# Optimization experiments

Measured on AMD Instinct MI355X. Metric: run time of the kernel, lower is better.

The kernel has to match this reference:

```python
import jax, jax.numpy as jnp
import numpy as np

C = 256
CQK = C // 8


def setup_inputs() -> dict:
    key = jax.random.key(0)
    ks = jax.random.split(key, 8)
    B, H, W = 4, 64, 64
    inputs = jax.random.normal(ks[0], (B, H, W, C), dtype=jnp.float32)
    s = 1.0 / np.sqrt(C)
    Wq = jax.random.normal(ks[1], (C, CQK), dtype=jnp.float32) * s
    bq = jnp.zeros((CQK,), dtype=jnp.float32)
    Wk = jax.random.normal(ks[2], (C, CQK), dtype=jnp.float32) * s
    bk = jnp.zeros((CQK,), dtype=jnp.float32)
    Wv = jax.random.normal(ks[3], (C, C), dtype=jnp.float32) * s
    bv = jnp.zeros((C,), dtype=jnp.float32)
    gamma = jnp.float32(0.7)  # nonzero so attention branch contributes
    return {"inputs": inputs, "Wq": Wq, "bq": bq, "Wk": Wk, "bk": bk,
            "Wv": Wv, "bv": bv, "gamma": gamma}


def reference(inputs, Wq, bq, Wk, bk, Wv, bv, gamma):
    B, H, W, Cin = inputs.shape
    N = H * W
    x = inputs.reshape(B, N, Cin)
    # 1x1 convs == per-pixel channel matmuls
    q = x @ Wq + bq                      # (B, N, C//8)
    k = x @ Wk + bk                      # (B, N, C//8)
    v = x @ Wv + bv                      # (B, N, C)
    energy = jnp.einsum('bnd,bmd->bnm', q, k)   # (B, N, N), no scale (faithful)
    attn = jax.nn.softmax(energy, axis=-1)
    x_out = jnp.einsum('bnm,bmc->bnc', attn, v)  # (B, N, C)
    out = gamma * x_out.reshape(B, H, W, Cin) + inputs
    return out
```

## Files before the change

### kernel.cpp

```cpp
#include <hip/hip_runtime.h>
#include <hip/hip_bf16.h>

#define B_ 4
#define N_ 4096
#define C_ 256
#define D_ 32
#define LOG2E 1.44269504088896340736f

typedef __attribute__((ext_vector_type(8))) short short8;
typedef __attribute__((ext_vector_type(4))) short short4v;
typedef __attribute__((ext_vector_type(4))) float float4v;

__device__ inline short f2bf_rne(float f) {
  unsigned u = __builtin_bit_cast(unsigned, f);
  u += 0x7FFFu + ((u >> 16) & 1u);
  return (short)(u >> 16);
}

__device__ inline float fast_exp2(float x) { return __builtin_amdgcn_exp2f(x); }

__global__ __launch_bounds__(256) void cast_w_kernel(
    const float* __restrict__ Wq, const float* __restrict__ Wk,
    const float* __restrict__ Wv, short* __restrict__ WtF) {
  int i  = blockIdx.x * 256 + threadIdx.x;
  int j  = i & 7;
  int l  = (i >> 3) & 63;
  int ks = (i >> 9) & 7;
  int nb = i >> 12;
  int n  = nb * 16 + (l & 15);
  int k  = ks * 32 + ((l >> 4) << 3) + j;
  float v;
  if (n < 32)      v = Wq[k * 32 + n] * LOG2E;
  else if (n < 64) v = Wk[k * 32 + (n - 32)];
  else             v = Wv[k * 256 + (n - 64)];
  WtF[i] = f2bf_rne(v);
}

__global__ __launch_bounds__(256, 2) void proj_kernel(
    const float* __restrict__ x, const short* __restrict__ WtF,
    const float* __restrict__ bq, const float* __restrict__ bk,
    const float* __restrict__ bv,
    short* __restrict__ qb, short* __restrict__ kF, short* __restrict__ vF) {
  int blk = blockIdx.x;
  int b  = blk >> 7;
  int r0 = (blk & 127) * 32;
  int t  = threadIdx.x;
  int w  = t >> 6;
  int l  = t & 63;
  int lc = l & 15;
  int q4 = l >> 4;

  __shared__ __align__(16) short sA[32][272];
  __shared__ __align__(16) short sV[256][40];
  __shared__ __align__(16) short sK[32][36];

  {
    const float* xb = x + (size_t)(b * N_ + r0) * C_;
#pragma unroll
    for (int ch = 0; ch < 8; ch++) {
      int f   = ch * 256 + t;
      int row = f >> 6;
      int col = (f & 63) * 4;
      float4v v = *(const float4v*)(xb + f * 4);
      short4v s;
      s[0] = f2bf_rne(v[0]); s[1] = f2bf_rne(v[1]);
      s[2] = f2bf_rne(v[2]); s[3] = f2bf_rne(v[3]);
      *(short4v*)(&sA[row][col]) = s;
    }
  }
  __syncthreads();

  float4v acc[10];
#pragma unroll
  for (int i = 0; i < 10; i++) { acc[i][0] = 0.f; acc[i][1] = 0.f; acc[i][2] = 0.f; acc[i][3] = 0.f; }

#pragma unroll
  for (int ks = 0; ks < 8; ks++) {
    short8 af0 = *(const short8*)(&sA[lc][ks * 32 + q4 * 8]);
    short8 af1 = *(const short8*)(&sA[16 + lc][ks * 32 + q4 * 8]);
#pragma unroll
    for (int nbo = 0; nbo < 5; nbo++) {
      int nb = w * 5 + nbo;
      short8 bf = *(const short8*)(WtF + (((nb << 3) + ks) << 9) + l * 8);
      acc[nbo * 2 + 0] = __builtin_amdgcn_mfma_f32_16x16x32_bf16(af0, bf, acc[nbo * 2 + 0], 0, 0, 0);
      acc[nbo * 2 + 1] = __builtin_amdgcn_mfma_f32_16x16x32_bf16(af1, bf, acc[nbo * 2 + 1], 0, 0, 0);
    }
  }

#pragma unroll
  for (int nbo = 0; nbo < 5; nbo++) {
    int n = (w * 5 + nbo) * 16 + lc;
    float bias = (n < 32) ? bq[n] * LOG2E : (n < 64) ? bk[n - 32] : bv[n - 64];
#pragma unroll
    for (int rt = 0; rt < 2; rt++) {
#pragma unroll
      for (int r = 0; r < 4; r++) {
        int row = rt * 16 + q4 * 4 + r;
        short s = f2bf_rne(acc[nbo * 2 + rt][r] + bias);
        if (n < 32)      qb[(size_t)(b * N_ + r0 + row) * D_ + n] = s;
        else if (n < 64) sK[row][n - 32] = s;
        else             sV[n - 64][row] = s;
      }
    }
  }
  __syncthreads();

  int kt  = r0 >> 6;
  int ks0 = (r0 >> 5) & 1;

  {
    int c = t;
    size_t tb = ((size_t)(b * 64 + kt) * 32 + ks0 * 16 + (c >> 4)) * 512;
#pragma unroll
    for (int rg = 0; rg < 4; rg++) {
      short8 vv = *(const short8*)(&sV[c][rg * 8]);
      *(short8*)(vF + tb + (rg * 16 + (c & 15)) * 8) = vv;
    }
  }
  if (t < 128) {
    int row = t >> 2, dg = t & 3;
    size_t tb = ((size_t)(b * 64 + kt) * 4 + ks0 * 2 + (row >> 4)) * 512;
    short8 kv = *(const short8*)(&sK[row][dg * 8]);
    *(short8*)(kF + tb + (dg * 16 + (row & 15)) * 8) = kv;
  }
}

__global__ __launch_bounds__(512, 2) void flash_kernel(
    const short* __restrict__ qb, const short* __restrict__ kF,
    const short* __restrict__ vF, const float* __restrict__ xin,
    const float* __restrict__ gptr, float* __restrict__ out) {
  int blk = blockIdx.x;
  int b  = blk & 3;
  int qt = (blk >> 3) * 2 + ((blk >> 2) & 1);
  int r0 = qt * 64;
  int t  = threadIdx.x;
  int w  = t >> 6;
  int l  = t & 63;
  int lc = l & 15;
  int q4 = l >> 4;
  int rq = w & 3;
  int h  = w >> 2;

  __shared__ __align__(16) short sP[8][16][36];
  __shared__ __align__(16) float4v mbuf[2][16][64];
  __shared__ float sLh[64];
  __shared__ float sLm[64];

  short8 qf = *(const short8*)(qb + (size_t)(b * N_ + r0 + rq * 16 + lc) * D_ + q4 * 8);

  const short* kp = kF + (size_t)b * (64 * 4 * 512) + h * (2 * 512) + l * 8;
  const short* vp = vF + (size_t)b * (64 * 32 * 512) + h * (16 * 512) + l * 8;

  short8 vA[16], vB[16];
  short8 kX0, kX1, kY0, kY1;

  kX0 = *(const short8*)(kp);
  kX1 = *(const short8*)(kp + 512);
#pragma unroll
  for (int cb = 0; cb < 16; cb++)
    vA[cb] = *(const short8*)(vp + cb * 512);

  float4v O[16];
#pragma unroll
  for (int i = 0; i < 16; i++) { O[i][0] = 0.f; O[i][1] = 0.f; O[i][2] = 0.f; O[i][3] = 0.f; }
  float l_part = 0.f;

  short (*sPw)[36] = sP[w];

#define TILE_PHASE(KC0, KC1, KP0, KP1, VCUR, VNXT, TI)                          \
  {                                                                             \
    int nt = ((TI) + 1 < 64) ? (TI) + 1 : 63;                                   \
    _Pragma("unroll")                                                           \
    for (int cb = 0; cb < 16; cb++)                                             \
      VNXT[cb] = *(const short8*)(vp + (size_t)nt * (32 * 512) + cb * 512);     \
    KP0 = *(const short8*)(kp + (size_t)nt * (4 * 512));                        \
    KP1 = *(const short8*)(kp + (size_t)nt * (4 * 512) + 512);                  \
    float4v z; z[0] = 0.f; z[1] = 0.f; z[2] = 0.f; z[3] = 0.f;                  \
    float4v St0 = __builtin_amdgcn_mfma_f32_16x16x32_bf16(KC0, qf, z, 0, 0, 0); \
    float4v St1 = __builtin_amdgcn_mfma_f32_16x16x32_bf16(KC1, qf, z, 0, 0, 0); \
    float p0 = fast_exp2(St0[0]), p1 = fast_exp2(St0[1]);                       \
    float p2 = fast_exp2(St0[2]), p3 = fast_exp2(St0[3]);                       \
    float p4 = fast_exp2(St1[0]), p5 = fast_exp2(St1[1]);                       \
    float p6 = fast_exp2(St1[2]), p7 = fast_exp2(St1[3]);                       \
    l_part += ((p0 + p1) + (p2 + p3)) + ((p4 + p5) + (p6 + p7));                \
    short4v pk0, pk1;                                                           \
    pk0[0] = f2bf_rne(p0); pk0[1] = f2bf_rne(p1);                               \
    pk0[2] = f2bf_rne(p2); pk0[3] = f2bf_rne(p3);                               \
    pk1[0] = f2bf_rne(p4); pk1[1] = f2bf_rne(p5);                               \
    pk1[2] = f2bf_rne(p6); pk1[3] = f2bf_rne(p7);                               \
    *(short4v*)(&sPw[lc][q4 * 4]) = pk0;                                        \
    *(short4v*)(&sPw[lc][16 + q4 * 4]) = pk1;                                   \
    short8 pf = *(const short8*)(&sPw[lc][q4 * 8]);                             \
    _Pragma("unroll")                                                           \
    for (int cb = 0; cb < 16; cb++)                                             \
      O[cb] = __builtin_amdgcn_mfma_f32_16x16x32_bf16(pf, VCUR[cb], O[cb], 0, 0, 0); \
  }

  for (int kt = 0; kt < 64; kt += 2) {
    TILE_PHASE(kX0, kX1, kY0, kY1, vA, vB, kt);
    TILE_PHASE(kY0, kY1, kX0, kX1, vB, vA, kt + 1);
  }
#undef TILE_PHASE

  float l_tot = l_part + __shfl_xor(l_part, 16, 64);
  l_tot += __shfl_xor(l_tot, 32, 64);
  bool lo = (h == 0);
  if (!lo && q4 == 0) sLh[rq * 16 + lc] = l_tot;
  __syncthreads();
  if (lo && q4 == 0) sLm[rq * 16 + lc] = l_tot + sLh[rq * 16 + lc];

  if (w == 4 || w == 5) {
#pragma unroll
    for (int cb = 0; cb < 16; cb++) mbuf[w - 4][cb][l] = O[cb];
  }
  __syncthreads();
  if (w == 0 || w == 1) {
#pragma unroll
    for (int cb = 0; cb < 16; cb++) {
      float4v m = mbuf[w][cb][l];
      O[cb][0] += m[0]; O[cb][1] += m[1]; O[cb][2] += m[2]; O[cb][3] += m[3];
    }
  }
  __syncthreads();
  if (w == 6 || w == 7) {
#pragma unroll
    for (int cb = 0; cb < 16; cb++) mbuf[w - 6][cb][l] = O[cb];
  }
  __syncthreads();
  if (w == 2 || w == 3) {
#pragma unroll
    for (int cb = 0; cb < 16; cb++) {
      float4v m = mbuf[w - 2][cb][l];
      O[cb][0] += m[0]; O[cb][1] += m[1]; O[cb][2] += m[2]; O[cb][3] += m[3];
    }
  }

  if (lo) {
    float g = *gptr;
    float4v lv = *(const float4v*)(&sLm[rq * 16 + q4 * 4]);
    float4v inv;
#pragma unroll
    for (int r = 0; r < 4; r++) inv[r] = __builtin_amdgcn_rcpf(lv[r]);
#pragma unroll
    for (int cb = 0; cb < 16; cb++) {
#pragma unroll
      for (int r = 0; r < 4; r++) {
        size_t idx = (size_t)(b * N_ + r0 + rq * 16 + q4 * 4 + r) * C_ + cb * 16 + lc;
        out[idx] = g * (O[cb][r] * inv[r]) + xin[idx];
      }
    }
  }
}

extern "C" void kernel_launch(void* const* d_in, const int* in_sizes, int n_in,
                              void* d_out, int out_size, void* d_ws, size_t ws_size,
                              hipStream_t stream) {
  const float* x     = (const float*)d_in[0];
  const float* Wq    = (const float*)d_in[1];
  const float* bq    = (const float*)d_in[2];
  const float* Wk    = (const float*)d_in[3];
  const float* bk    = (const float*)d_in[4];
  const float* Wv    = (const float*)d_in[5];
  const float* bv    = (const float*)d_in[6];
  const float* gamma = (const float*)d_in[7];
  float* out = (float*)d_out;

  char* ws = (char*)d_ws;
  short* qb  = (short*)ws;
  short* kF  = (short*)(ws + (1u << 20));
  short* vF  = (short*)(ws + (2u << 20));
  short* WtF = (short*)(ws + (10u << 20));

  hipLaunchKernelGGL(cast_w_kernel, dim3(320), dim3(256), 0, stream, Wq, Wk, Wv, WtF);
  hipLaunchKernelGGL(proj_kernel,   dim3(512), dim3(256), 0, stream, x, WtF, bq, bk, bv, qb, kF, vF);
  hipLaunchKernelGGL(flash_kernel,  dim3(256), dim3(512), 0, stream, qb, kF, vF, x, gamma, out);
}
```

Baseline: 164.6 us.

## Split flash attention over key halves with partial outputs and a merge kernel

Restructures attention so each block handles a 64-query tile over half of the keys. Score computation is shared through a double-buffered LDS P tile by four waves, while eight waves split the V columns and key sub-blocks. Partial outputs and row sums go to workspace in bf16, and a new merge kernel combines the halves and applies gamma plus the residual. This doubles the grid and cuts per-thread V register prefetch so occupancy can rise (launch bounds raised to 4). The cost is an extra kernel launch, a global round-trip of the partials, per-tile block barriers, and bf16 rounding of intermediate sums. It also reorders the proj_kernel column-block assignment per wave.

```diff
diff --git a/kernel.cpp b/kernel.cpp
--- a/kernel.cpp
+++ b/kernel.cpp
@@ -16,7 +16,10 @@
   u += 0x7FFFu + ((u >> 16) & 1u);
   return (short)(u >> 16);
 }
-
+__device__ inline float bf2f(short s) {
+  unsigned u = ((unsigned)(unsigned short)s) << 16;
+  return __builtin_bit_cast(float, u);
+}
 __device__ inline float fast_exp2(float x) { return __builtin_amdgcn_exp2f(x); }
 
 __global__ __launch_bounds__(256) void cast_w_kernel(
@@ -36,7 +39,7 @@
   WtF[i] = f2bf_rne(v);
 }
 
-__global__ __launch_bounds__(256, 2) void proj_kernel(
+__global__ __launch_bounds__(256, 4) void proj_kernel(
     const float* __restrict__ x, const short* __restrict__ WtF,
     const float* __restrict__ bq, const float* __restrict__ bk,
     const float* __restrict__ bv,
@@ -80,7 +83,7 @@
     short8 af1 = *(const short8*)(&sA[16 + lc][ks * 32 + q4 * 8]);
 #pragma unroll
     for (int nbo = 0; nbo < 5; nbo++) {
-      int nb = w * 5 + nbo;
+      int nb = nbo * 4 + w;
       short8 bf = *(const short8*)(WtF + (((nb << 3) + ks) << 9) + l * 8);
       acc[nbo * 2 + 0] = __builtin_amdgcn_mfma_f32_16x16x32_bf16(af0, bf, acc[nbo * 2 + 0], 0, 0, 0);
       acc[nbo * 2 + 1] = __builtin_amdgcn_mfma_f32_16x16x32_bf16(af1, bf, acc[nbo * 2 + 1], 0, 0, 0);
@@ -89,17 +92,21 @@
 
 #pragma unroll
   for (int nbo = 0; nbo < 5; nbo++) {
-    int n = (w * 5 + nbo) * 16 + lc;
-    float bias = (n < 32) ? bq[n] * LOG2E : (n < 64) ? bk[n - 32] : bv[n - 64];
+    float bias;
+    if (nbo == 0) bias = (w < 2) ? bq[w * 16 + lc] * LOG2E : bk[(w - 2) * 16 + lc];
+    else          bias = bv[(nbo - 1) * 64 + w * 16 + lc];
 #pragma unroll
     for (int rt = 0; rt < 2; rt++) {
 #pragma unroll
       for (int r = 0; r < 4; r++) {
         int row = rt * 16 + q4 * 4 + r;
         short s = f2bf_rne(acc[nbo * 2 + rt][r] + bias);
-        if (n < 32)      qb[(size_t)(b * N_ + r0 + row) * D_ + n] = s;
-        else if (n < 64) sK[row][n - 32] = s;
-        else             sV[n - 64][row] = s;
+        if (nbo == 0) {
+          if (w < 2) qb[(size_t)(b * N_ + r0 + row) * D_ + w * 16 + lc] = s;
+          else       sK[row][(w - 2) * 16 + lc] = s;
+        } else {
+          sV[(nbo - 1) * 64 + w * 16 + lc][row] = s;
+        }
       }
     }
   }
@@ -125,13 +132,14 @@
   }
 }
 
-__global__ __launch_bounds__(512, 2) void flash_kernel(
+__global__ __launch_bounds__(512, 4) void flash_partial_kernel(
     const short* __restrict__ qb, const short* __restrict__ kF,
-    const short* __restrict__ vF, const float* __restrict__ xin,
-    const float* __restrict__ gptr, float* __restrict__ out) {
+    const short* __restrict__ vF, short* __restrict__ obuf,
+    float* __restrict__ lbuf) {
   int blk = blockIdx.x;
   int b  = blk & 3;
-  int qt = (blk >> 3) * 2 + ((blk >> 2) & 1);
+  int hb = (blk >> 2) & 1;
+  int qt = blk >> 3;
   int r0 = qt * 64;
   int t  = threadIdx.x;
   int w  = t >> 6;
@@ -139,116 +147,184 @@
   int lc = l & 15;
   int q4 = l >> 4;
   int rq = w & 3;
-  int h  = w >> 2;
-
-  __shared__ __align__(16) short sP[8][16][36];
-  __shared__ __align__(16) float4v mbuf[2][16][64];
-  __shared__ float sLh[64];
-  __shared__ float sLm[64];
+  int kh = w >> 2;
+  int cq = w & 3;
+
+  __shared__ __align__(16) short sP[2][64][72];
+
+  int p = (b * 64 + qt) * 2 + hb;
 
   short8 qf = *(const short8*)(qb + (size_t)(b * N_ + r0 + rq * 16 + lc) * D_ + q4 * 8);
 
-  const short* kp = kF + (size_t)b * (64 * 4 * 512) + h * (2 * 512) + l * 8;
-  const short* vp = vF + (size_t)b * (64 * 32 * 512) + h * (16 * 512) + l * 8;
-
-  short8 vA[16], vB[16];
-  short8 kX0, kX1, kY0, kY1;
-
-  kX0 = *(const short8*)(kp);
-  kX1 = *(const short8*)(kp + 512);
-#pragma unroll
-  for (int cb = 0; cb < 16; cb++)
-    vA[cb] = *(const short8*)(vp + cb * 512);
+  const short* kpb = kF + ((size_t)(b * 64 + hb * 32) * 4) * 512 + l * 8;
+  const short* vpb = vF + ((size_t)(b * 64 + hb * 32) * 32 + kh * 16 + cq * 4) * 512 + l * 8;
+
+  short8 kr0, kr1, kr2, kr3;
+  short8 vr0, vr1, vr2, vr3;
+  kr0 = *(const short8*)(kpb + 0 * 512);
+  kr1 = *(const short8*)(kpb + 1 * 512);
+  kr2 = *(const short8*)(kpb + 2 * 512);
+  kr3 = *(const short8*)(kpb + 3 * 512);
+  vr0 = *(const short8*)(vpb + 0 * 512);
+  vr1 = *(const short8*)(vpb + 1 * 512);
+  vr2 = *(const short8*)(vpb + 2 * 512);
+  vr3 = *(const short8*)(vpb + 3 * 512);
 
   float4v O[16];
 #pragma unroll
   for (int i = 0; i < 16; i++) { O[i][0] = 0.f; O[i][1] = 0.f; O[i][2] = 0.f; O[i][3] = 0.f; }
   float l_part = 0.f;
 
-  short (*sPw)[36] = sP[w];
-
-#define TILE_PHASE(KC0, KC1, KP0, KP1, VCUR, VNXT, TI)                          \
-  {                                                                             \
-    int nt = ((TI) + 1 < 64) ? (TI) + 1 : 63;                                   \
-    _Pragma("unroll")                                                           \
-    for (int cb = 0; cb < 16; cb++)                                             \
-      VNXT[cb] = *(const short8*)(vp + (size_t)nt * (32 * 512) + cb * 512);     \
-    KP0 = *(const short8*)(kp + (size_t)nt * (4 * 512));                        \
-    KP1 = *(const short8*)(kp + (size_t)nt * (4 * 512) + 512);                  \
-    float4v z; z[0] = 0.f; z[1] = 0.f; z[2] = 0.f; z[3] = 0.f;                  \
-    float4v St0 = __builtin_amdgcn_mfma_f32_16x16x32_bf16(KC0, qf, z, 0, 0, 0); \
-    float4v St1 = __builtin_amdgcn_mfma_f32_16x16x32_bf16(KC1, qf, z, 0, 0, 0); \
-    float p0 = fast_exp2(St0[0]), p1 = fast_exp2(St0[1]);                       \
-    float p2 = fast_exp2(St0[2]), p3 = fast_exp2(St0[3]);                       \
-    float p4 = fast_exp2(St1[0]), p5 = fast_exp2(St1[1]);                       \
-    float p6 = fast_exp2(St1[2]), p7 = fast_exp2(St1[3]);                       \
-    l_part += ((p0 + p1) + (p2 + p3)) + ((p4 + p5) + (p6 + p7));                \
-    short4v pk0, pk1;                                                           \
-    pk0[0] = f2bf_rne(p0); pk0[1] = f2bf_rne(p1);                               \
-    pk0[2] = f2bf_rne(p2); pk0[3] = f2bf_rne(p3);                               \
-    pk1[0] = f2bf_rne(p4); pk1[1] = f2bf_rne(p5);                               \
-    pk1[2] = f2bf_rne(p6); pk1[3] = f2bf_rne(p7);                               \
-    *(short4v*)(&sPw[lc][q4 * 4]) = pk0;                                        \
-    *(short4v*)(&sPw[lc][16 + q4 * 4]) = pk1;                                   \
-    short8 pf = *(const short8*)(&sPw[lc][q4 * 8]);                             \
-    _Pragma("unroll")                                                           \
-    for (int cb = 0; cb < 16; cb++)                                             \
-      O[cb] = __builtin_amdgcn_mfma_f32_16x16x32_bf16(pf, VCUR[cb], O[cb], 0, 0, 0); \
-  }
-
-  for (int kt = 0; kt < 64; kt += 2) {
-    TILE_PHASE(kX0, kX1, kY0, kY1, vA, vB, kt);
-    TILE_PHASE(kY0, kY1, kX0, kX1, vB, vA, kt + 1);
-  }
-#undef TILE_PHASE
-
-  float l_tot = l_part + __shfl_xor(l_part, 16, 64);
-  l_tot += __shfl_xor(l_tot, 32, 64);
-  bool lo = (h == 0);
-  if (!lo && q4 == 0) sLh[rq * 16 + lc] = l_tot;
-  __syncthreads();
-  if (lo && q4 == 0) sLm[rq * 16 + lc] = l_tot + sLh[rq * 16 + lc];
-
+  for (int ti = 0; ti < 32; ti++) {
+    short* sPb = &sP[ti & 1][0][0];
+    size_t nto = (size_t)((ti + 1 < 32) ? ti + 1 : 31);
+
+    if (w < 4) {
+      float4v z; z[0] = 0.f; z[1] = 0.f; z[2] = 0.f; z[3] = 0.f;
+      float4v St0 = __builtin_amdgcn_mfma_f32_16x16x32_bf16(kr0, qf, z, 0, 0, 0);
+      float4v St1 = __builtin_amdgcn_mfma_f32_16x16x32_bf16(kr1, qf, z, 0, 0, 0);
+      float4v St2 = __builtin_amdgcn_mfma_f32_16x16x32_bf16(kr2, qf, z, 0, 0, 0);
+      float4v St3 = __builtin_amdgcn_mfma_f32_16x16x32_bf16(kr3, qf, z, 0, 0, 0);
+      kr0 = *(const short8*)(kpb + nto * 2048 + 0 * 512);
+      kr1 = *(const short8*)(kpb + nto * 2048 + 1 * 512);
+      kr2 = *(const short8*)(kpb + nto * 2048 + 2 * 512);
+      kr3 = *(const short8*)(kpb + nto * 2048 + 3 * 512);
+      short* rowp = sPb + (rq * 16 + lc) * 72 + q4 * 4;
+      float ts;
+      {
+        float p0 = fast_exp2(St0[0]), p1 = fast_exp2(St0[1]);
+        float p2 = fast_exp2(St0[2]), p3 = fast_exp2(St0[3]);
+        ts = (p0 + p1) + (p2 + p3);
+        short4v pk; pk[0] = f2bf_rne(p0); pk[1] = f2bf_rne(p1);
+        pk[2] = f2bf_rne(p2); pk[3] = f2bf_rne(p3);
+        *(short4v*)(rowp + 0) = pk;
+      }
+      {
+        float p0 = fast_exp2(St1[0]), p1 = fast_exp2(St1[1]);
+        float p2 = fast_exp2(St1[2]), p3 = fast_exp2(St1[3]);
+        ts += (p0 + p1) + (p2 + p3);
+        short4v pk; pk[0] = f2bf_rne(p0); pk[1] = f2bf_rne(p1);
+        pk[2] = f2bf_rne(p2); pk[3] = f2bf_rne(p3);
+        *(short4v*)(rowp + 16) = pk;
+      }
+      {
+        float p0 = fast_exp2(St2[0]), p1 = fast_exp2(St2[1]);
+        float p2 = fast_exp2(St2[2]), p3 = fast_exp2(St2[3]);
+        ts += (p0 + p1) + (p2 + p3);
+        short4v pk; pk[0] = f2bf_rne(p0); pk[1] = f2bf_rne(p1);
+        pk[2] = f2bf_rne(p2); pk[3] = f2bf_rne(p3);
+        *(short4v*)(rowp + 32) = pk;
+      }
+      {
+        float p0 = fast_exp2(St3[0]), p1 = fast_exp2(St3[1]);
+        float p2 = fast_exp2(St3[2]), p3 = fast_exp2(St3[3]);
+        ts += (p0 + p1) + (p2 + p3);
+        short4v pk; pk[0] = f2bf_rne(p0); pk[1] = f2bf_rne(p1);
+        pk[2] = f2bf_rne(p2); pk[3] = f2bf_rne(p3);
+        *(short4v*)(rowp + 48) = pk;
+      }
+      l_part += ts;
+    }
+
+    __syncthreads();
+
+#pragma unroll
+    for (int rt = 0; rt < 4; rt++) {
+      short8 pf = *(const short8*)(sPb + (rt * 16 + lc) * 72 + kh * 32 + q4 * 8);
+      O[rt * 4 + 0] = __builtin_amdgcn_mfma_f32_16x16x32_bf16(pf, vr0, O[rt * 4 + 0], 0, 0, 0);
+      O[rt * 4 + 1] = __builtin_amdgcn_mfma_f32_16x16x32_bf16(pf, vr1, O[rt * 4 + 1], 0, 0, 0);
+      O[rt * 4 + 2] = __builtin_amdgcn_mfma_f32_16x16x32_bf16(pf, vr2, O[rt * 4 + 2], 0, 0, 0);
+      O[rt * 4 + 3] = __builtin_amdgcn_mfma_f32_16x16x32_bf16(pf, vr3, O[rt * 4 + 3], 0, 0, 0);
+    }
+    vr0 = *(const short8*)(vpb + nto * 16384 + 0 * 512);
+    vr1 = *(const short8*)(vpb + nto * 16384 + 1 * 512);
+    vr2 = *(const short8*)(vpb + nto * 16384 + 2 * 512);
+    vr3 = *(const short8*)(vpb + nto * 16384 + 3 * 512);
+  }
+
+  __syncthreads();
+  short* lds16 = &sP[0][0][0];
   if (w == 4 || w == 5) {
-#pragma unroll
-    for (int cb = 0; cb < 16; cb++) mbuf[w - 4][cb][l] = O[cb];
+    int slot = w - 4;
+#pragma unroll
+    for (int f = 0; f < 16; f++)
+#pragma unroll
+      for (int r = 0; r < 4; r++)
+        lds16[((slot * 16 + f) * 4 + r) * 64 + l] = f2bf_rne(O[f][r]);
   }
   __syncthreads();
   if (w == 0 || w == 1) {
 #pragma unroll
-    for (int cb = 0; cb < 16; cb++) {
-      float4v m = mbuf[w][cb][l];
-      O[cb][0] += m[0]; O[cb][1] += m[1]; O[cb][2] += m[2]; O[cb][3] += m[3];
-    }
+    for (int f = 0; f < 16; f++)
+#pragma unroll
+      for (int r = 0; r < 4; r++)
+        O[f][r] += bf2f(lds16[((w * 16 + f) * 4 + r) * 64 + l]);
   }
   __syncthreads();
   if (w == 6 || w == 7) {
-#pragma unroll
-    for (int cb = 0; cb < 16; cb++) mbuf[w - 6][cb][l] = O[cb];
+    int slot = w - 6;
+#pragma unroll
+    for (int f = 0; f < 16; f++)
+#pragma unroll
+      for (int r = 0; r < 4; r++)
+        lds16[((slot * 16 + f) * 4 + r) * 64 + l] = f2bf_rne(O[f][r]);
   }
   __syncthreads();
   if (w == 2 || w == 3) {
 #pragma unroll
-    for (int cb = 0; cb < 16; cb++) {
-      float4v m = mbuf[w - 2][cb][l];
-      O[cb][0] += m[0]; O[cb][1] += m[1]; O[cb][2] += m[2]; O[cb][3] += m[3];
-    }
-  }
-
-  if (lo) {
-    float g = *gptr;
-    float4v lv = *(const float4v*)(&sLm[rq * 16 + q4 * 4]);
-    float4v inv;
-#pragma unroll
-    for (int r = 0; r < 4; r++) inv[r] = __builtin_amdgcn_rcpf(lv[r]);
-#pragma unroll
-    for (int cb = 0; cb < 16; cb++) {
-#pragma unroll
-      for (int r = 0; r < 4; r++) {
-        size_t idx = (size_t)(b * N_ + r0 + rq * 16 + q4 * 4 + r) * C_ + cb * 16 + lc;
-        out[idx] = g * (O[cb][r] * inv[r]) + xin[idx];
-      }
-    }
+    for (int f = 0; f < 16; f++)
+#pragma unroll
+      for (int r = 0; r < 4; r++)
+        O[f][r] += bf2f(lds16[(((w - 2) * 16 + f) * 4 + r) * 64 + l]);
+  }
+
+  if (w < 4) {
+    short* ob = obuf + (size_t)p * (64 * 256);
+#pragma unroll
+    for (int rt = 0; rt < 4; rt++)
+#pragma unroll
+      for (int cb = 0; cb < 4; cb++)
+#pragma unroll
+        for (int r = 0; r < 4; r++)
+          ob[(rt * 16 + q4 * 4 + r) * 256 + cq * 64 + cb * 16 + lc] =
+              f2bf_rne(O[rt * 4 + cb][r]);
+    float l_tot = l_part + __shfl_xor(l_part, 16, 64);
+    l_tot += __shfl_xor(l_tot, 32, 64);
+    if (l < 16) lbuf[(size_t)p * 64 + rq * 16 + l] = l_tot;
+  }
+}
+
+__global__ __launch_bounds__(256) void merge_kernel(
+    const short* __restrict__ obuf, const float* __restrict__ lbuf,
+    const float* __restrict__ xin, const float* __restrict__ gptr,
+    float* __restrict__ out) {
+  int blk = blockIdx.x;
+  int t   = threadIdx.x;
+  float g = *gptr;
+  const short* o0 = obuf + (size_t)(blk * 2 + 0) * 16384;
+  const short* o1 = obuf + (size_t)(blk * 2 + 1) * 16384;
+  const float* l0 = lbuf + (size_t)(blk * 2 + 0) * 64;
+  const float* l1 = lbuf + (size_t)(blk * 2 + 1) * 64;
+  size_t gbase = (size_t)blk * 16384;
+#pragma unroll
+  for (int i = 0; i < 8; i++) {
+    int j   = i * 256 + t;
+    int row = j >> 5;
+    short8 a = *(const short8*)(o0 + j * 8);
+    short8 c = *(const short8*)(o1 + j * 8);
+    float linv = __builtin_amdgcn_rcpf(l0[row] + l1[row]);
+    size_t gi = gbase + (size_t)j * 8;
+    float4v x0 = *(const float4v*)(xin + gi);
+    float4v x1 = *(const float4v*)(xin + gi + 4);
+    float4v r0v, r1v;
+#pragma unroll
+    for (int e = 0; e < 4; e++)
+      r0v[e] = g * ((bf2f(a[e]) + bf2f(c[e])) * linv) + x0[e];
+#pragma unroll
+    for (int e = 0; e < 4; e++)
+      r1v[e] = g * ((bf2f(a[e + 4]) + bf2f(c[e + 4])) * linv) + x1[e];
+    *(float4v*)(out + gi)     = r0v;
+    *(float4v*)(out + gi + 4) = r1v;
   }
 }
 
@@ -266,12 +342,15 @@
   float* out = (float*)d_out;
 
   char* ws = (char*)d_ws;
-  short* qb  = (short*)ws;
-  short* kF  = (short*)(ws + (1u << 20));
-  short* vF  = (short*)(ws + (2u << 20));
-  short* WtF = (short*)(ws + (10u << 20));
-
-  hipLaunchKernelGGL(cast_w_kernel, dim3(320), dim3(256), 0, stream, Wq, Wk, Wv, WtF);
-  hipLaunchKernelGGL(proj_kernel,   dim3(512), dim3(256), 0, stream, x, WtF, bq, bk, bv, qb, kF, vF);
-  hipLaunchKernelGGL(flash_kernel,  dim3(256), dim3(512), 0, stream, qb, kF, vF, x, gamma, out);
-}
+  short* qb   = (short*)ws;
+  short* kF   = (short*)(ws + (1u << 20));
+  short* vF   = (short*)(ws + (2u << 20));
+  short* WtF  = (short*)(ws + (10u << 20));
+  short* obuf = (short*)(ws + (11u << 20));
+  float* lbuf = (float*)(ws + (28u << 20));
+
+  hipLaunchKernelGGL(cast_w_kernel,      dim3(320), dim3(256), 0, stream, Wq, Wk, Wv, WtF);
+  hipLaunchKernelGGL(proj_kernel,        dim3(512), dim3(256), 0, stream, x, WtF, bq, bk, bv, qb, kF, vF);
+  hipLaunchKernelGGL(flash_partial_kernel, dim3(512), dim3(512), 0, stream, qb, kF, vF, obuf, lbuf);
+  hipLaunchKernelGGL(merge_kernel,       dim3(256), dim3(256), 0, stream, obuf, lbuf, x, gamma, out);
+}
```

After: 157.3 us. 1.05x faster.

## Split flash attention over key halves with separate merge kernel

Applied to the files above, without the earlier changes.

The flash kernel is restructured so each block handles one key half for a 64-query tile, giving 512 blocks instead of 256. Within a block, four waves compute QK and exp into a double-buffered shared P tile while all eight waves do PV on a channel slice, so register demand drops and occupancy rises. Partial outputs are written in bf16 along with row sums, and a new merge kernel combines the two halves, normalizes and adds the residual. The proj kernel also gets a different column-block assignment per wave and a higher occupancy hint. The trade-offs are extra global traffic for the bf16 partials, an additional kernel launch, a barrier per tile, and an added bf16 rounding of the partial outputs.

```diff
diff --git a/kernel.cpp b/kernel.cpp
--- a/kernel.cpp
+++ b/kernel.cpp
@@ -6,6 +6,7 @@
 #define C_ 256
 #define D_ 32
 #define LOG2E 1.44269504088896340736f
+#define MFMA16 __builtin_amdgcn_mfma_f32_16x16x32_bf16
 
 typedef __attribute__((ext_vector_type(8))) short short8;
 typedef __attribute__((ext_vector_type(4))) short short4v;
@@ -16,7 +17,10 @@
   u += 0x7FFFu + ((u >> 16) & 1u);
   return (short)(u >> 16);
 }
-
+__device__ inline float bf2f(short s) {
+  unsigned u = ((unsigned)(unsigned short)s) << 16;
+  return __builtin_bit_cast(float, u);
+}
 __device__ inline float fast_exp2(float x) { return __builtin_amdgcn_exp2f(x); }
 
 __global__ __launch_bounds__(256) void cast_w_kernel(
@@ -36,7 +40,7 @@
   WtF[i] = f2bf_rne(v);
 }
 
-__global__ __launch_bounds__(256, 2) void proj_kernel(
+__global__ __launch_bounds__(256, 4) void proj_kernel(
     const float* __restrict__ x, const short* __restrict__ WtF,
     const float* __restrict__ bq, const float* __restrict__ bk,
     const float* __restrict__ bv,
@@ -80,26 +84,30 @@
     short8 af1 = *(const short8*)(&sA[16 + lc][ks * 32 + q4 * 8]);
 #pragma unroll
     for (int nbo = 0; nbo < 5; nbo++) {
-      int nb = w * 5 + nbo;
+      int nb = nbo * 4 + w;
       short8 bf = *(const short8*)(WtF + (((nb << 3) + ks) << 9) + l * 8);
-      acc[nbo * 2 + 0] = __builtin_amdgcn_mfma_f32_16x16x32_bf16(af0, bf, acc[nbo * 2 + 0], 0, 0, 0);
-      acc[nbo * 2 + 1] = __builtin_amdgcn_mfma_f32_16x16x32_bf16(af1, bf, acc[nbo * 2 + 1], 0, 0, 0);
+      acc[nbo * 2 + 0] = MFMA16(af0, bf, acc[nbo * 2 + 0], 0, 0, 0);
+      acc[nbo * 2 + 1] = MFMA16(af1, bf, acc[nbo * 2 + 1], 0, 0, 0);
     }
   }
 
 #pragma unroll
   for (int nbo = 0; nbo < 5; nbo++) {
-    int n = (w * 5 + nbo) * 16 + lc;
-    float bias = (n < 32) ? bq[n] * LOG2E : (n < 64) ? bk[n - 32] : bv[n - 64];
+    float bias;
+    if (nbo == 0) bias = (w < 2) ? bq[w * 16 + lc] * LOG2E : bk[(w - 2) * 16 + lc];
+    else          bias = bv[(nbo - 1) * 64 + w * 16 + lc];
 #pragma unroll
     for (int rt = 0; rt < 2; rt++) {
 #pragma unroll
       for (int r = 0; r < 4; r++) {
         int row = rt * 16 + q4 * 4 + r;
         short s = f2bf_rne(acc[nbo * 2 + rt][r] + bias);
-        if (n < 32)      qb[(size_t)(b * N_ + r0 + row) * D_ + n] = s;
-        else if (n < 64) sK[row][n - 32] = s;
-        else             sV[n - 64][row] = s;
+        if (nbo == 0) {
+          if (w < 2) qb[(size_t)(b * N_ + r0 + row) * D_ + w * 16 + lc] = s;
+          else       sK[row][(w - 2) * 16 + lc] = s;
+        } else {
+          sV[(nbo - 1) * 64 + w * 16 + lc][row] = s;
+        }
       }
     }
   }
@@ -125,13 +133,14 @@
   }
 }
 
-__global__ __launch_bounds__(512, 2) void flash_kernel(
+__global__ __launch_bounds__(512, 4) void flash_partial_kernel(
     const short* __restrict__ qb, const short* __restrict__ kF,
-    const short* __restrict__ vF, const float* __restrict__ xin,
-    const float* __restrict__ gptr, float* __restrict__ out) {
+    const short* __restrict__ vF, short* __restrict__ obuf,
+    float* __restrict__ lbuf) {
   int blk = blockIdx.x;
   int b  = blk & 3;
-  int qt = (blk >> 3) * 2 + ((blk >> 2) & 1);
+  int hb = (blk >> 2) & 1;
+  int qt = blk >> 3;
   int r0 = qt * 64;
   int t  = threadIdx.x;
   int w  = t >> 6;
@@ -139,115 +148,183 @@
   int lc = l & 15;
   int q4 = l >> 4;
   int rq = w & 3;
-  int h  = w >> 2;
-
-  __shared__ __align__(16) short sP[8][16][36];
-  __shared__ __align__(16) float4v mbuf[2][16][64];
-  __shared__ float sLh[64];
-  __shared__ float sLm[64];
+  bool qkw = (w < 4);
+
+  __shared__ __align__(16) short sP[2][64][72];
+
+  int p = (b * 64 + qt) * 2 + hb;
 
   short8 qf = *(const short8*)(qb + (size_t)(b * N_ + r0 + rq * 16 + lc) * D_ + q4 * 8);
 
-  const short* kp = kF + (size_t)b * (64 * 4 * 512) + h * (2 * 512) + l * 8;
-  const short* vp = vF + (size_t)b * (64 * 32 * 512) + h * (16 * 512) + l * 8;
-
-  short8 vA[16], vB[16];
-  short8 kX0, kX1, kY0, kY1;
-
-  kX0 = *(const short8*)(kp);
-  kX1 = *(const short8*)(kp + 512);
-#pragma unroll
-  for (int cb = 0; cb < 16; cb++)
-    vA[cb] = *(const short8*)(vp + cb * 512);
-
-  float4v O[16];
-#pragma unroll
-  for (int i = 0; i < 16; i++) { O[i][0] = 0.f; O[i][1] = 0.f; O[i][2] = 0.f; O[i][3] = 0.f; }
+  const short* kbp = kF + ((size_t)(b * 64 + hb * 32) * 4) * 512 + l * 8;
+  const short* vbp = vF + ((size_t)(b * 64 + hb * 32) * 32 + 2 * w) * 512 + l * 8;
+
+  short8 kC0, kC1, kC2, kC3;
+  short8 vX00, vX01, vX10, vX11;
+  short8 vY00, vY01, vY10, vY11;
+
+  kC0 = *(const short8*)(kbp + 0);
+  kC1 = *(const short8*)(kbp + 512);
+  kC2 = *(const short8*)(kbp + 1024);
+  kC3 = *(const short8*)(kbp + 1536);
+  vX00 = *(const short8*)(vbp + 0);
+  vX01 = *(const short8*)(vbp + 512);
+  vX10 = *(const short8*)(vbp + 8192);
+  vX11 = *(const short8*)(vbp + 8704);
+
+  float4v O[8];
+#pragma unroll
+  for (int i = 0; i < 8; i++) { O[i][0] = 0.f; O[i][1] = 0.f; O[i][2] = 0.f; O[i][3] = 0.f; }
   float l_part = 0.f;
 
-  short (*sPw)[36] = sP[w];
-
-#define TILE_PHASE(KC0, KC1, KP0, KP1, VCUR, VNXT, TI)                          \
-  {                                                                             \
-    int nt = ((TI) + 1 < 64) ? (TI) + 1 : 63;                                   \
-    _Pragma("unroll")                                                           \
-    for (int cb = 0; cb < 16; cb++)                                             \
-      VNXT[cb] = *(const short8*)(vp + (size_t)nt * (32 * 512) + cb * 512);     \
-    KP0 = *(const short8*)(kp + (size_t)nt * (4 * 512));                        \
-    KP1 = *(const short8*)(kp + (size_t)nt * (4 * 512) + 512);                  \
-    float4v z; z[0] = 0.f; z[1] = 0.f; z[2] = 0.f; z[3] = 0.f;                  \
-    float4v St0 = __builtin_amdgcn_mfma_f32_16x16x32_bf16(KC0, qf, z, 0, 0, 0); \
-    float4v St1 = __builtin_amdgcn_mfma_f32_16x16x32_bf16(KC1, qf, z, 0, 0, 0); \
-    float p0 = fast_exp2(St0[0]), p1 = fast_exp2(St0[1]);                       \
-    float p2 = fast_exp2(St0[2]), p3 = fast_exp2(St0[3]);                       \
-    float p4 = fast_exp2(St1[0]), p5 = fast_exp2(St1[1]);                       \
-    float p6 = fast_exp2(St1[2]), p7 = fast_exp2(St1[3]);                       \
-    l_part += ((p0 + p1) + (p2 + p3)) + ((p4 + p5) + (p6 + p7));                \
-    short4v pk0, pk1;                                                           \
-    pk0[0] = f2bf_rne(p0); pk0[1] = f2bf_rne(p1);                               \
-    pk0[2] = f2bf_rne(p2); pk0[3] = f2bf_rne(p3);                               \
-    pk1[0] = f2bf_rne(p4); pk1[1] = f2bf_rne(p5);                               \
-    pk1[2] = f2bf_rne(p6); pk1[3] = f2bf_rne(p7);                               \
-    *(short4v*)(&sPw[lc][q4 * 4]) = pk0;                                        \
-    *(short4v*)(&sPw[lc][16 + q4 * 4]) = pk1;                                   \
-    short8 pf = *(const short8*)(&sPw[lc][q4 * 8]);                             \
-    _Pragma("unroll")                                                           \
-    for (int cb = 0; cb < 16; cb++)                                             \
-      O[cb] = __builtin_amdgcn_mfma_f32_16x16x32_bf16(pf, VCUR[cb], O[cb], 0, 0, 0); \
-  }
-
-  for (int kt = 0; kt < 64; kt += 2) {
-    TILE_PHASE(kX0, kX1, kY0, kY1, vA, vB, kt);
-    TILE_PHASE(kY0, kY1, kX0, kX1, vB, vA, kt + 1);
-  }
-#undef TILE_PHASE
-
-  float l_tot = l_part + __shfl_xor(l_part, 16, 64);
-  l_tot += __shfl_xor(l_tot, 32, 64);
-  bool lo = (h == 0);
-  if (!lo && q4 == 0) sLh[rq * 16 + lc] = l_tot;
+#define K_RELOAD(TI)                                                           \
+  { size_t o_ = (size_t)(TI) * 2048;                                           \
+    kC0 = *(const short8*)(kbp + o_);                                          \
+    kC1 = *(const short8*)(kbp + o_ + 512);                                    \
+    kC2 = *(const short8*)(kbp + o_ + 1024);                                   \
+    kC3 = *(const short8*)(kbp + o_ + 1536); }
+
+#define QK_STEP(SPB, VALID)                                                    \
+  { float4v z; z[0] = 0.f; z[1] = 0.f; z[2] = 0.f; z[3] = 0.f;                 \
+    float4v S0 = MFMA16(kC0, qf, z, 0, 0, 0);                                  \
+    float4v S1 = MFMA16(kC1, qf, z, 0, 0, 0);                                  \
+    float4v S2 = MFMA16(kC2, qf, z, 0, 0, 0);                                  \
+    float4v S3 = MFMA16(kC3, qf, z, 0, 0, 0);                                  \
+    short* rowp = &sP[SPB][rq * 16 + lc][q4 * 4];                              \
+    float ts = 0.f;                                                            \
+    { float p0 = fast_exp2(S0[0]), p1 = fast_exp2(S0[1]);                      \
+      float p2 = fast_exp2(S0[2]), p3 = fast_exp2(S0[3]);                      \
+      ts += (p0 + p1) + (p2 + p3);                                             \
+      short4v pk; pk[0] = f2bf_rne(p0); pk[1] = f2bf_rne(p1);                  \
+      pk[2] = f2bf_rne(p2); pk[3] = f2bf_rne(p3);                              \
+      *(short4v*)(rowp + 0) = pk; }                                            \
+    { float p0 = fast_exp2(S1[0]), p1 = fast_exp2(S1[1]);                      \
+      float p2 = fast_exp2(S1[2]), p3 = fast_exp2(S1[3]);                      \
+      ts += (p0 + p1) + (p2 + p3);                                             \
+      short4v pk; pk[0] = f2bf_rne(p0); pk[1] = f2bf_rne(p1);                  \
+      pk[2] = f2bf_rne(p2); pk[3] = f2bf_rne(p3);                              \
+      *(short4v*)(rowp + 16) = pk; }                                           \
+    { float p0 = fast_exp2(S2[0]), p1 = fast_exp2(S2[1]);                      \
+      float p2 = fast_exp2(S2[2]), p3 = fast_exp2(S2[3]);                      \
+      ts += (p0 + p1) + (p2 + p3);                                             \
+      short4v pk; pk[0] = f2bf_rne(p0); pk[1] = f2bf_rne(p1);                  \
+      pk[2] = f2bf_rne(p2); pk[3] = f2bf_rne(p3);                              \
+      *(short4v*)(rowp + 32) = pk; }                                           \
+    { float p0 = fast_exp2(S3[0]), p1 = fast_exp2(S3[1]);                      \
+      float p2 = fast_exp2(S3[2]), p3 = fast_exp2(S3[3]);                      \
+      ts += (p0 + p1) + (p2 + p3);                                             \
+      short4v pk; pk[0] = f2bf_rne(p0); pk[1] = f2bf_rne(p1);                  \
+      pk[2] = f2bf_rne(p2); pk[3] = f2bf_rne(p3);                              \
+      *(short4v*)(rowp + 48) = pk; }                                           \
+    if (VALID) l_part += ts; }
+
+#define PV_STEP(SPB, V00, V01, V10, V11)                                       \
+  { _Pragma("unroll")                                                          \
+    for (int rt = 0; rt < 4; rt++) {                                           \
+      short8 pf0 = *(const short8*)(&sP[SPB][rt * 16 + lc][q4 * 8]);           \
+      short8 pf1 = *(const short8*)(&sP[SPB][rt * 16 + lc][32 + q4 * 8]);      \
+      O[rt * 2 + 0] = MFMA16(pf0, V00, O[rt * 2 + 0], 0, 0, 0);                \
+      O[rt * 2 + 0] = MFMA16(pf1, V10, O[rt * 2 + 0], 0, 0, 0);                \
+      O[rt * 2 + 1] = MFMA16(pf0, V01, O[rt * 2 + 1], 0, 0, 0);                \
+      O[rt * 2 + 1] = MFMA16(pf1, V11, O[rt * 2 + 1], 0, 0, 0);                \
+    } }
+
+  if (qkw) {
+    QK_STEP(0, true)
+    K_RELOAD(1)
+  }
   __syncthreads();
-  if (lo && q4 == 0) sLm[rq * 16 + lc] = l_tot + sLh[rq * 16 + lc];
-
-  if (w == 4 || w == 5) {
-#pragma unroll
-    for (int cb = 0; cb < 16; cb++) mbuf[w - 4][cb][l] = O[cb];
-  }
-  __syncthreads();
-  if (w == 0 || w == 1) {
-#pragma unroll
-    for (int cb = 0; cb < 16; cb++) {
-      float4v m = mbuf[w][cb][l];
-      O[cb][0] += m[0]; O[cb][1] += m[1]; O[cb][2] += m[2]; O[cb][3] += m[3];
-    }
-  }
-  __syncthreads();
-  if (w == 6 || w == 7) {
-#pragma unroll
-    for (int cb = 0; cb < 16; cb++) mbuf[w - 6][cb][l] = O[cb];
-  }
-  __syncthreads();
-  if (w == 2 || w == 3) {
-#pragma unroll
-    for (int cb = 0; cb < 16; cb++) {
-      float4v m = mbuf[w - 2][cb][l];
-      O[cb][0] += m[0]; O[cb][1] += m[1]; O[cb][2] += m[2]; O[cb][3] += m[3];
-    }
-  }
-
-  if (lo) {
-    float g = *gptr;
-    float4v lv = *(const float4v*)(&sLm[rq * 16 + q4 * 4]);
-    float4v inv;
-#pragma unroll
-    for (int r = 0; r < 4; r++) inv[r] = __builtin_amdgcn_rcpf(lv[r]);
-#pragma unroll
-    for (int cb = 0; cb < 16; cb++) {
-#pragma unroll
-      for (int r = 0; r < 4; r++) {
-        size_t idx = (size_t)(b * N_ + r0 + rq * 16 + q4 * 4 + r) * C_ + cb * 16 + lc;
-        out[idx] = g * (O[cb][r] * inv[r]) + xin[idx];
-      }
+
+  for (int ti = 0; ti < 32; ti += 2) {
+    int n1 = ti + 1;
+    int n2 = (ti + 2 < 32) ? ti + 2 : 31;
+    bool v2 = (ti + 2 < 32);
+    int n3 = (ti + 3 < 32) ? ti + 3 : 31;
+
+    { size_t vo = (size_t)n1 * 16384;
+      vY00 = *(const short8*)(vbp + vo);
+      vY01 = *(const short8*)(vbp + vo + 512);
+      vY10 = *(const short8*)(vbp + vo + 8192);
+      vY11 = *(const short8*)(vbp + vo + 8704); }
+    if (qkw) {
+      QK_STEP(1, true)
+      K_RELOAD(n2)
+    }
+    PV_STEP(0, vX00, vX01, vX10, vX11)
+    __syncthreads();
+
+    { size_t vo = (size_t)n2 * 16384;
+      vX00 = *(const short8*)(vbp + vo);
+      vX01 = *(const short8*)(vbp + vo + 512);
+      vX10 = *(const short8*)(vbp + vo + 8192);
+      vX11 = *(const short8*)(vbp + vo + 8704); }
+    if (qkw) {
+      QK_STEP(0, v2)
+      K_RELOAD(n3)
+    }
+    PV_STEP(1, vY00, vY01, vY10, vY11)
+    __syncthreads();
+  }
+#undef K_RELOAD
+#undef QK_STEP
+#undef PV_STEP
+
+  {
+    short* ob = obuf + ((size_t)p * 64 + w * 8) * 256 + l * 4;
+#pragma unroll
+    for (int a = 0; a < 8; a++) {
+      float4v o = O[a];
+      short4v pk;
+      pk[0] = f2bf_rne(o[0]); pk[1] = f2bf_rne(o[1]);
+      pk[2] = f2bf_rne(o[2]); pk[3] = f2bf_rne(o[3]);
+      *(short4v*)(ob + a * 256) = pk;
+    }
+  }
+  if (qkw) {
+    float l_tot = l_part + __shfl_xor(l_part, 16, 64);
+    l_tot += __shfl_xor(l_tot, 32, 64);
+    if (q4 == 0) lbuf[(size_t)p * 64 + rq * 16 + lc] = l_tot;
+  }
+}
+
+__global__ __launch_bounds__(256) void merge_kernel(
+    const short* __restrict__ obuf, const float* __restrict__ lbuf,
+    const float* __restrict__ xin, const float* __restrict__ gptr,
+    float* __restrict__ out) {
+  int blk = blockIdx.x;
+  int t   = threadIdx.x;
+  int s   = t >> 2;
+  int qr  = t & 3;
+  int wv  = s >> 3, j = s & 7, rt = j >> 1, cbo = j & 1;
+  int chb = wv * 32 + cbo * 16;
+  float g = *gptr;
+
+  const short* o0 = obuf + ((size_t)(blk * 2 + 0) * 64 + s) * 256 + qr * 64;
+  const short* o1 = obuf + ((size_t)(blk * 2 + 1) * 64 + s) * 256 + qr * 64;
+  const float* l0 = lbuf + (size_t)(blk * 2 + 0) * 64;
+  const float* l1 = lbuf + (size_t)(blk * 2 + 1) * 64;
+
+  short4v a[16], c[16];
+#pragma unroll
+  for (int i = 0; i < 16; i++) {
+    a[i] = ((const short4v*)o0)[i];
+    c[i] = ((const short4v*)o1)[i];
+  }
+
+  size_t rowbase = (size_t)blk * 64;
+#pragma unroll
+  for (int r = 0; r < 4; r++) {
+    int q = rt * 16 + qr * 4 + r;
+    float linv = __builtin_amdgcn_rcpf(l0[q] + l1[q]);
+    size_t gi = (rowbase + q) * C_ + chb;
+#pragma unroll
+    for (int i0 = 0; i0 < 16; i0 += 4) {
+      float4v xv = *(const float4v*)(xin + gi + i0);
+      float4v ov;
+#pragma unroll
+      for (int e = 0; e < 4; e++)
+        ov[e] = g * ((bf2f(a[i0 + e][r]) + bf2f(c[i0 + e][r])) * linv) + xv[e];
+      *(float4v*)(out + gi + i0) = ov;
     }
   }
 }
@@ -266,12 +343,15 @@
   float* out = (float*)d_out;
 
   char* ws = (char*)d_ws;
-  short* qb  = (short*)ws;
-  short* kF  = (short*)(ws + (1u << 20));
-  short* vF  = (short*)(ws + (2u << 20));
-  short* WtF = (short*)(ws + (10u << 20));
-
-  hipLaunchKernelGGL(cast_w_kernel, dim3(320), dim3(256), 0, stream, Wq, Wk, Wv, WtF);
-  hipLaunchKernelGGL(proj_kernel,   dim3(512), dim3(256), 0, stream, x, WtF, bq, bk, bv, qb, kF, vF);
-  hipLaunchKernelGGL(flash_kernel,  dim3(256), dim3(512), 0, stream, qb, kF, vF, x, gamma, out);
-}
+  short* qb   = (short*)ws;
+  short* kF   = (short*)(ws + (1u << 20));
+  short* vF   = (short*)(ws + (2u << 20));
+  short* WtF  = (short*)(ws + (10u << 20));
+  short* obuf = (short*)(ws + (11u << 20));
+  float* lbuf = (float*)(ws + (28u << 20));
+
+  hipLaunchKernelGGL(cast_w_kernel,        dim3(320), dim3(256), 0, stream, Wq, Wk, Wv, WtF);
+  hipLaunchKernelGGL(proj_kernel,          dim3(512), dim3(256), 0, stream, x, WtF, bq, bk, bv, qb, kF, vF);
+  hipLaunchKernelGGL(flash_partial_kernel, dim3(512), dim3(512), 0, stream, qb, kF, vF, obuf, lbuf);
+  hipLaunchKernelGGL(merge_kernel,         dim3(256), dim3(256), 0, stream, obuf, lbuf, x, gamma, out);
+}
```

New measurement: 147.7 us. -10.2%, faster.
